# Performance work log

Measured on AMD Instinct MI355X. Metric: run time of the kernel, lower is better.

Reference implementation:

```python
import jax, jax.numpy as jnp
import numpy as np

IOU_THRESHOLD = 0.5  # default iou_threshold of nms/class_spec_nms


def _nms_keep_mask(boxes, scores, iou_threshold):
    """Faithful port of the hand-rolled greedy NMS.

    The torch version builds a variable-length index list; here we return the
    equivalent fixed-shape boolean keep mask over the N boxes (jit-friendly).
    """
    n = scores.shape[0]
    x1, y1, x2, y2 = boxes[:, 0], boxes[:, 1], boxes[:, 2], boxes[:, 3]
    areas = (x2 - x1) * (y2 - y1)                       # [N]
    # pairwise intersection via broadcasted min/max (same math as the matmul-
    # with-ones trick in the source, without materializing the ones matrices)
    xi = jnp.minimum(x2[:, None], x2[None, :]) - jnp.maximum(x1[:, None], x1[None, :])
    yi = jnp.minimum(y2[:, None], y2[None, :]) - jnp.maximum(y1[:, None], y1[None, :])
    inter = jnp.maximum(xi, 0.0) * jnp.maximum(yi, 0.0)  # [N,N]
    iou = inter / (areas[:, None] + areas[None, :] - inter)

    first_max = scores.max()
    first_min = scores.min()
    curr_idx0 = jnp.argmax(scores)

    # carry: (candidate mask, working scores copy, keep mask, curr max, curr idx)
    init = (scores < first_max, scores, jnp.zeros((n,), dtype=bool), first_max, curr_idx0)

    def cond(state):
        mask, _, _, cmax, _ = state
        return jnp.any(mask) & (cmax >= first_min)

    def body(state):
        mask, sc, keep, cmax, cidx = state
        mask = mask & (iou[cidx] <= iou_threshold)   # suppress overlaps with current max
        mask = mask.at[cidx].set(False)
        keep = keep.at[cidx].set(True)               # keep current max
        sc = jnp.where(mask, sc, first_min - 1.0)    # kill suppressed scores
        cidx = jnp.argmax(sc)
        return mask, sc, keep, sc[cidx], cidx

    _, _, keep, _, _ = jax.lax.while_loop(cond, body, init)
    return keep


def setup_inputs() -> dict:
    key = jax.random.key(0)
    k1, k2, k3, k4, k5, k6 = jax.random.split(key, 6)
    N = 4096    # pre-NMS candidate boxes
    L = 16384   # p3 locations for a 1024x1024 image at stride 8 (128*128)
    xy = jax.random.uniform(k1, (N, 2), dtype=jnp.float32) * 900.0
    wh = jax.random.uniform(k2, (N, 2), dtype=jnp.float32) * 100.0 + 1.0
    boxes = jnp.concatenate([xy, xy + wh], axis=1)          # valid x1<x2, y1<y2
    scores = jax.random.uniform(k3, (N,), dtype=jnp.float32)
    class_ids = jax.random.randint(k4, (N,), 0, 80, dtype=jnp.int32)
    locations = jax.random.uniform(k5, (L, 2), dtype=jnp.float32) * 1024.0
    deltas = jax.random.uniform(k6, (L, 4), dtype=jnp.float32)  # positive gt deltas
    return {"boxes": boxes, "scores": scores, "class_ids": class_ids,
            "locations": locations, "deltas": deltas, "stride": 8}


def reference(boxes, scores, class_ids, locations, deltas, stride):
    # ---- class_spec_nms: class-offset trick then plain NMS ----
    max_coordinate = boxes.max()
    offsets = class_ids.astype(boxes.dtype) * (max_coordinate + 1.0)
    boxes_for_nms = boxes + offsets[:, None]
    keep_mask = _nms_keep_mask(boxes_for_nms, scores, IOU_THRESHOLD)

    # ---- fcos_apply_deltas_to_locations ----
    clipped = jnp.maximum(deltas, 0.0)
    s = jnp.asarray(stride, dtype=deltas.dtype)
    px, py = locations[:, 0], locations[:, 1]
    pred_boxes = jnp.stack([px - clipped[:, 0] * s,
                            py - clipped[:, 1] * s,
                            px + clipped[:, 2] * s,
                            py + clipped[:, 3] * s], axis=1)  # [L,4]

    # ---- fcos_make_centerness_targets ----
    lr_min = jnp.minimum(deltas[:, 0], deltas[:, 2])
    tb_min = jnp.minimum(deltas[:, 1], deltas[:, 3])
    lr_max = jnp.maximum(deltas[:, 0], deltas[:, 2])
    tb_max = jnp.maximum(deltas[:, 1], deltas[:, 3])
    centerness = jnp.sqrt((lr_min * tb_min) / (lr_max * tb_max))
    centerness = jnp.where(jnp.all(deltas == -1.0, axis=1), -1.0, centerness)

    pred_out = jnp.concatenate([pred_boxes, centerness[:, None]], axis=1)  # [L,5]
    return keep_mask, pred_out
```

## Files before the change

### kernel.cpp

```cpp
#include <hip/hip_runtime.h>
#include <stdint.h>

#define NB 4096
#define NBLK 64
#define LLOC 16384
#define IOU_THR 0.5f
#define ECAP 1024
#define RANKB 256
#define NTRI (NBLK * (NBLK + 1) / 2)

typedef unsigned long long u64;

__device__ __forceinline__ u64 readlane64(u64 v, int lane) {
    unsigned lo = (unsigned)__builtin_amdgcn_readlane((int)(unsigned)(v & 0xffffffffull), lane);
    unsigned hi = (unsigned)__builtin_amdgcn_readlane((int)(unsigned)(v >> 32), lane);
    return ((u64)hi << 32) | (u64)lo;
}

__global__ void __launch_bounds__(256) fused_front(
        const float* __restrict__ boxes, const float* __restrict__ scores,
        const float* __restrict__ loc, const float* __restrict__ deltas,
        const int* __restrict__ stride_p,
        float* __restrict__ pred_out, float* __restrict__ maxc,
        int* __restrict__ sidx, int* __restrict__ counts) {
    __shared__ __align__(16) float sh[NB];
    __shared__ float red[4];
    int blk = blockIdx.x;
    int t = threadIdx.x;

    if (blk < 64) {
        int i = blk * 256 + t;
        float s = (float)stride_p[0];
        float2 p = ((const float2*)loc)[i];
        float4 d = ((const float4*)deltas)[i];
        float c0 = fmaxf(d.x, 0.f), c1 = fmaxf(d.y, 0.f);
        float c2 = fmaxf(d.z, 0.f), c3 = fmaxf(d.w, 0.f);
        float b0 = p.x - c0 * s;
        float b1 = p.y - c1 * s;
        float b2 = p.x + c2 * s;
        float b3 = p.y + c3 * s;
        float lr_min = fminf(d.x, d.z), tb_min = fminf(d.y, d.w);
        float lr_max = fmaxf(d.x, d.z), tb_max = fmaxf(d.y, d.w);
        float cent = sqrtf((lr_min * tb_min) / (lr_max * tb_max));
        if (d.x == -1.f && d.y == -1.f && d.z == -1.f && d.w == -1.f) cent = -1.f;
        float* o = pred_out + (size_t)i * 5;
        o[0] = b0; o[1] = b1; o[2] = b2; o[3] = b3; o[4] = cent;
    } else if (blk < 64 + RANKB) {
        for (int i = t; i < NB; i += 256) sh[i] = scores[i];
        __syncthreads();
        int wave = t >> 6, lane = t & 63;
        int base = (blk - 64) * 16 + wave * 4;
        float my0 = sh[base + 0], my1 = sh[base + 1];
        float my2 = sh[base + 2], my3 = sh[base + 3];
        int c0 = 0, c1 = 0, c2 = 0, c3 = 0;
#pragma unroll 8
        for (int k = 0; k < 64; ++k) {
            int j = lane + k * 64;
            float sj = sh[j];
            c0 += (sj > my0) || (sj == my0 && j < base + 0);
            c1 += (sj > my1) || (sj == my1 && j < base + 1);
            c2 += (sj > my2) || (sj == my2 && j < base + 2);
            c3 += (sj > my3) || (sj == my3 && j < base + 3);
        }
        for (int o = 32; o > 0; o >>= 1) {
            c0 += __shfl_down(c0, o); c1 += __shfl_down(c1, o);
            c2 += __shfl_down(c2, o); c3 += __shfl_down(c3, o);
        }
        if (lane == 0) {
            sidx[c0] = base + 0; sidx[c1] = base + 1;
            sidx[c2] = base + 2; sidx[c3] = base + 3;
        }
    } else {
        if (t < NBLK) counts[t] = 0;
        float m = -3.0e38f;
        for (int i = t; i < NB * 4; i += 256) m = fmaxf(m, boxes[i]);
        for (int o = 32; o > 0; o >>= 1) m = fmaxf(m, __shfl_down(m, o));
        if ((t & 63) == 0) red[t >> 6] = m;
        __syncthreads();
        if (t == 0) *maxc = fmaxf(fmaxf(red[0], red[1]), fmaxf(red[2], red[3]));
    }
}

__global__ void __launch_bounds__(64) edge_kernel(
        const float* __restrict__ boxes, const int* __restrict__ cls,
        const float* __restrict__ maxc, const int* __restrict__ sidx,
        int* __restrict__ counts, uint4* __restrict__ entries) {
    int idx = blockIdx.x, r = 0;
    while (idx >= NBLK - r) { idx -= NBLK - r; ++r; }
    int c = r + idx;

    __shared__ float4 cb[64];
    __shared__ float ca[64];
    int t = threadIdx.x;
    float mc1 = maxc[0] + 1.0f;

    int jr = sidx[r * 64 + t];
    float offr = (float)cls[jr] * mc1;
    float4 rb = ((const float4*)boxes)[jr];
    rb.x += offr; rb.y += offr; rb.z += offr; rb.w += offr;
    float ra = (rb.z - rb.x) * (rb.w - rb.y);

    if (c == r) {
        cb[t] = rb; ca[t] = ra;
    } else {
        int jc = sidx[c * 64 + t];
        float offc = (float)cls[jc] * mc1;
        float4 b = ((const float4*)boxes)[jc];
        b.x += offc; b.y += offc; b.z += offc; b.w += offc;
        cb[t] = b; ca[t] = (b.z - b.x) * (b.w - b.y);
    }
    __syncthreads();

    u64 w = 0;
#pragma unroll 8
    for (int j = 0; j < 64; ++j) {
        float4 b = cb[j];
        float xi = fminf(rb.z, b.z) - fmaxf(rb.x, b.x);
        float yi = fminf(rb.w, b.w) - fmaxf(rb.y, b.y);
        float inter = fmaxf(xi, 0.f) * fmaxf(yi, 0.f);
        float iou = inter / (ra + ca[j] - inter);
        w |= (u64)(iou > IOU_THR) << j;
    }
    if (c == r) w &= ~(1ull << t);
    if (w) {
        int slot = atomicAdd(&counts[r], 1);
        if (slot < ECAP)
            entries[r * ECAP + slot] =
                make_uint4((unsigned)(t | (c << 8)), 0u,
                           (unsigned)(w & 0xffffffffull), (unsigned)(w >> 32));
    }
}

__global__ void __launch_bounds__(64) scan_kernel(
        const int* __restrict__ counts, const uint4* __restrict__ entries,
        const int* __restrict__ sidx, float* __restrict__ keep_out) {
    const int lane = threadIdx.x;
    int cnt_l = counts[lane];
    u64 accv = 0;
    u64 keptall = 0;
    u64 self = 1ull << lane;

    uint4 cur = entries[lane];
    uint4 n1  = entries[ECAP + lane];
    for (int b = 0; b < NBLK; ++b) {
        uint4 n2;
        if (b < NBLK - 2) n2 = entries[(u64)(b + 2) * ECAP + lane];

        int cnt = __builtin_amdgcn_readlane(cnt_l, b);
        if (cnt > ECAP) cnt = ECAP;
        int cfast = cnt < 64 ? cnt : 64;

        u64 colw = self;
        for (int e = 0; e < cfast; ++e) {
            unsigned meta = (unsigned)__builtin_amdgcn_readlane((int)cur.x, e);
            int l = meta & 255, c = meta >> 8;
            if (c == b) {
                unsigned lo = (unsigned)__builtin_amdgcn_readlane((int)cur.z, e);
                unsigned hi = (unsigned)__builtin_amdgcn_readlane((int)cur.w, e);
                if (lane == l) colw |= ((u64)hi << 32) | lo;
            }
        }
        for (int e = 64; e < cnt; ++e) {
            uint4 x = entries[(u64)b * ECAP + e];
            int l = x.x & 255, c = x.x >> 8;
            if (c == b && lane == l) colw |= ((u64)x.w << 32) | x.z;
        }

        u64 rem = readlane64(accv, b);
        u64 avail = ~rem;
        u64 edges = colw & avail & ~self;
        u64 involved = __ballot(edges != 0ull) & avail;
        u64 keptm = avail & ~involved;
        u64 sub = involved;
        while (sub) {
            int i = (int)__builtin_ctzll(sub);
            keptm |= 1ull << i;
            u64 ci = readlane64(colw, i);
            sub &= ~(ci | (1ull << i));
        }
        if (lane == b) keptall = keptm;

        for (int e = 0; e < cfast; ++e) {
            unsigned meta = (unsigned)__builtin_amdgcn_readlane((int)cur.x, e);
            unsigned lo   = (unsigned)__builtin_amdgcn_readlane((int)cur.z, e);
            unsigned hi   = (unsigned)__builtin_amdgcn_readlane((int)cur.w, e);
            int l = meta & 255, c = meta >> 8;
            if (((keptm >> l) & 1ull) && lane == c) accv |= ((u64)hi << 32) | lo;
        }
        for (int e = 64; e < cnt; ++e) {
            uint4 x = entries[(u64)b * ECAP + e];
            int l = x.x & 255, c = x.x >> 8;
            if (((keptm >> l) & 1ull) && lane == c) accv |= ((u64)x.w << 32) | x.z;
        }
        cur = n1; n1 = n2;
    }

#pragma unroll 8
    for (int bb = 0; bb < NBLK; ++bb) {
        u64 kw = readlane64(keptall, bb);
        int idx = sidx[bb * 64 + lane];
        keep_out[idx] = ((kw >> lane) & 1ull) ? 1.0f : 0.0f;
    }
}

extern "C" void kernel_launch(void* const* d_in, const int* in_sizes, int n_in,
                              void* d_out, int out_size, void* d_ws, size_t ws_size,
                              hipStream_t stream) {
    const float* boxes   = (const float*)d_in[0];
    const float* scores  = (const float*)d_in[1];
    const int*   cls     = (const int*)d_in[2];
    const float* loc     = (const float*)d_in[3];
    const float* deltas  = (const float*)d_in[4];
    const int*   stride  = (const int*)d_in[5];

    float* out = (float*)d_out;
    float* keep_out = out;
    float* pred_out = out + NB;

    char* ws = (char*)d_ws;
    float* maxc    = (float*)ws;                     ws += 16;
    int*   sidx    = (int*)ws;                       ws += NB * sizeof(int);
    int*   counts  = (int*)ws;                       ws += NBLK * sizeof(int) + 16;
    uint4* entries = (uint4*)ws;

    fused_front<<<64 + RANKB + 1, 256, 0, stream>>>(boxes, scores, loc, deltas, stride,
                                                    pred_out, maxc, sidx, counts);
    edge_kernel<<<NTRI, 64, 0, stream>>>(boxes, cls, maxc, sidx, counts, entries);
    scan_kernel<<<1, 64, 0, stream>>>(counts, entries, sidx, keep_out);
}
```

Baseline: 103.8 us.

## Fuse front, edge and scan kernels into one cooperative persistent kernel

The three separate launches (front/rank, pairwise IoU edge tiles, serial scan) are merged into one cooperative kernel with 256 blocks. Grid-wide syncs replace the kernel boundaries. The 2080 edge tiles are spread over the waves of the persistent grid in three rounds, and block 0 wave 0 runs the serial scan at the end. This removes two launch overheads and inter-kernel gaps, but adds grid.sync costs and leaves most of the grid idle during the scan phase.

```diff
diff --git a/kernel.cpp b/kernel.cpp
--- a/kernel.cpp
+++ b/kernel.cpp
@@ -1,13 +1,15 @@
 #include <hip/hip_runtime.h>
+#include <hip/hip_cooperative_groups.h>
 #include <stdint.h>
+
+namespace cg = cooperative_groups;
 
 #define NB 4096
 #define NBLK 64
-#define LLOC 16384
 #define IOU_THR 0.5f
 #define ECAP 1024
-#define RANKB 256
 #define NTRI (NBLK * (NBLK + 1) / 2)
+#define GRID 256
 
 typedef unsigned long long u64;
 
@@ -17,17 +19,48 @@
     return ((u64)hi << 32) | (u64)lo;
 }
 
-__global__ void __launch_bounds__(256) fused_front(
+__global__ void __launch_bounds__(256, 1) fcos_fused(
         const float* __restrict__ boxes, const float* __restrict__ scores,
-        const float* __restrict__ loc, const float* __restrict__ deltas,
-        const int* __restrict__ stride_p,
-        float* __restrict__ pred_out, float* __restrict__ maxc,
-        int* __restrict__ sidx, int* __restrict__ counts) {
+        const int* __restrict__ cls, const float* __restrict__ loc,
+        const float* __restrict__ deltas, const int* __restrict__ stride_p,
+        float* __restrict__ keep_out, float* __restrict__ pred_out,
+        float* __restrict__ maxc, int* __restrict__ sidx,
+        int* __restrict__ counts, uint4* __restrict__ entries) {
+    cg::grid_group grid = cg::this_grid();
     __shared__ __align__(16) float sh[NB];
     __shared__ float red[4];
-    int blk = blockIdx.x;
-    int t = threadIdx.x;
-
+    __shared__ float4 cbs[4][64];
+    __shared__ float  cas[4][64];
+
+    const int blk  = blockIdx.x;
+    const int t    = threadIdx.x;
+    const int wave = t >> 6, lane = t & 63;
+
+    {
+        for (int i = t; i < NB; i += 256) sh[i] = scores[i];
+        __syncthreads();
+        int base = blk * 16 + wave * 4;
+        float my0 = sh[base + 0], my1 = sh[base + 1];
+        float my2 = sh[base + 2], my3 = sh[base + 3];
+        int c0 = 0, c1 = 0, c2 = 0, c3 = 0;
+#pragma unroll 8
+        for (int k = 0; k < 64; ++k) {
+            int j = lane + k * 64;
+            float sj = sh[j];
+            c0 += (sj > my0) || (sj == my0 && j < base + 0);
+            c1 += (sj > my1) || (sj == my1 && j < base + 1);
+            c2 += (sj > my2) || (sj == my2 && j < base + 2);
+            c3 += (sj > my3) || (sj == my3 && j < base + 3);
+        }
+        for (int o = 32; o > 0; o >>= 1) {
+            c0 += __shfl_down(c0, o); c1 += __shfl_down(c1, o);
+            c2 += __shfl_down(c2, o); c3 += __shfl_down(c3, o);
+        }
+        if (lane == 0) {
+            sidx[c0] = base + 0; sidx[c1] = base + 1;
+            sidx[c2] = base + 2; sidx[c3] = base + 3;
+        }
+    }
     if (blk < 64) {
         int i = blk * 256 + t;
         float s = (float)stride_p[0];
@@ -45,32 +78,7 @@
         if (d.x == -1.f && d.y == -1.f && d.z == -1.f && d.w == -1.f) cent = -1.f;
         float* o = pred_out + (size_t)i * 5;
         o[0] = b0; o[1] = b1; o[2] = b2; o[3] = b3; o[4] = cent;
-    } else if (blk < 64 + RANKB) {
-        for (int i = t; i < NB; i += 256) sh[i] = scores[i];
-        __syncthreads();
-        int wave = t >> 6, lane = t & 63;
-        int base = (blk - 64) * 16 + wave * 4;
-        float my0 = sh[base + 0], my1 = sh[base + 1];
-        float my2 = sh[base + 2], my3 = sh[base + 3];
-        int c0 = 0, c1 = 0, c2 = 0, c3 = 0;
-#pragma unroll 8
-        for (int k = 0; k < 64; ++k) {
-            int j = lane + k * 64;
-            float sj = sh[j];
-            c0 += (sj > my0) || (sj == my0 && j < base + 0);
-            c1 += (sj > my1) || (sj == my1 && j < base + 1);
-            c2 += (sj > my2) || (sj == my2 && j < base + 2);
-            c3 += (sj > my3) || (sj == my3 && j < base + 3);
-        }
-        for (int o = 32; o > 0; o >>= 1) {
-            c0 += __shfl_down(c0, o); c1 += __shfl_down(c1, o);
-            c2 += __shfl_down(c2, o); c3 += __shfl_down(c3, o);
-        }
-        if (lane == 0) {
-            sidx[c0] = base + 0; sidx[c1] = base + 1;
-            sidx[c2] = base + 2; sidx[c3] = base + 3;
-        }
-    } else {
+    } else if (blk == 64) {
         if (t < NBLK) counts[t] = 0;
         float m = -3.0e38f;
         for (int i = t; i < NB * 4; i += 256) m = fmaxf(m, boxes[i]);
@@ -79,127 +87,128 @@
         __syncthreads();
         if (t == 0) *maxc = fmaxf(fmaxf(red[0], red[1]), fmaxf(red[2], red[3]));
     }
-}
-
-__global__ void __launch_bounds__(64) edge_kernel(
-        const float* __restrict__ boxes, const int* __restrict__ cls,
-        const float* __restrict__ maxc, const int* __restrict__ sidx,
-        int* __restrict__ counts, uint4* __restrict__ entries) {
-    int idx = blockIdx.x, r = 0;
-    while (idx >= NBLK - r) { idx -= NBLK - r; ++r; }
-    int c = r + idx;
-
-    __shared__ float4 cb[64];
-    __shared__ float ca[64];
-    int t = threadIdx.x;
+    __threadfence();
+    grid.sync();
+
     float mc1 = maxc[0] + 1.0f;
-
-    int jr = sidx[r * 64 + t];
-    float offr = (float)cls[jr] * mc1;
-    float4 rb = ((const float4*)boxes)[jr];
-    rb.x += offr; rb.y += offr; rb.z += offr; rb.w += offr;
-    float ra = (rb.z - rb.x) * (rb.w - rb.y);
-
-    if (c == r) {
-        cb[t] = rb; ca[t] = ra;
-    } else {
-        int jc = sidx[c * 64 + t];
-        float offc = (float)cls[jc] * mc1;
-        float4 b = ((const float4*)boxes)[jc];
-        b.x += offc; b.y += offc; b.z += offc; b.w += offc;
-        cb[t] = b; ca[t] = (b.z - b.x) * (b.w - b.y);
-    }
-    __syncthreads();
-
-    u64 w = 0;
+    for (int round = 0; round < 3; ++round) {
+        int tile = round * (GRID * 4) + blk * 4 + wave;
+        bool active = tile < NTRI;
+        int r = 0, cc = 0;
+        float4 rb; float ra = 0.f;
+        if (active) {
+            int idx = tile;
+            while (idx >= NBLK - r) { idx -= NBLK - r; ++r; }
+            cc = r + idx;
+            int jr = sidx[r * 64 + lane];
+            float offr = (float)cls[jr] * mc1;
+            rb = ((const float4*)boxes)[jr];
+            rb.x += offr; rb.y += offr; rb.z += offr; rb.w += offr;
+            ra = (rb.z - rb.x) * (rb.w - rb.y);
+            if (cc == r) {
+                cbs[wave][lane] = rb; cas[wave][lane] = ra;
+            } else {
+                int jc = sidx[cc * 64 + lane];
+                float offc = (float)cls[jc] * mc1;
+                float4 b = ((const float4*)boxes)[jc];
+                b.x += offc; b.y += offc; b.z += offc; b.w += offc;
+                cbs[wave][lane] = b;
+                cas[wave][lane] = (b.z - b.x) * (b.w - b.y);
+            }
+        }
+        __syncthreads();
+        if (active) {
+            u64 w = 0;
 #pragma unroll 8
-    for (int j = 0; j < 64; ++j) {
-        float4 b = cb[j];
-        float xi = fminf(rb.z, b.z) - fmaxf(rb.x, b.x);
-        float yi = fminf(rb.w, b.w) - fmaxf(rb.y, b.y);
-        float inter = fmaxf(xi, 0.f) * fmaxf(yi, 0.f);
-        float iou = inter / (ra + ca[j] - inter);
-        w |= (u64)(iou > IOU_THR) << j;
-    }
-    if (c == r) w &= ~(1ull << t);
-    if (w) {
-        int slot = atomicAdd(&counts[r], 1);
-        if (slot < ECAP)
-            entries[r * ECAP + slot] =
-                make_uint4((unsigned)(t | (c << 8)), 0u,
-                           (unsigned)(w & 0xffffffffull), (unsigned)(w >> 32));
-    }
-}
-
-__global__ void __launch_bounds__(64) scan_kernel(
-        const int* __restrict__ counts, const uint4* __restrict__ entries,
-        const int* __restrict__ sidx, float* __restrict__ keep_out) {
-    const int lane = threadIdx.x;
-    int cnt_l = counts[lane];
-    u64 accv = 0;
-    u64 keptall = 0;
-    u64 self = 1ull << lane;
-
-    uint4 cur = entries[lane];
-    uint4 n1  = entries[ECAP + lane];
-    for (int b = 0; b < NBLK; ++b) {
-        uint4 n2;
-        if (b < NBLK - 2) n2 = entries[(u64)(b + 2) * ECAP + lane];
-
-        int cnt = __builtin_amdgcn_readlane(cnt_l, b);
-        if (cnt > ECAP) cnt = ECAP;
-        int cfast = cnt < 64 ? cnt : 64;
-
-        u64 colw = self;
-        for (int e = 0; e < cfast; ++e) {
-            unsigned meta = (unsigned)__builtin_amdgcn_readlane((int)cur.x, e);
-            int l = meta & 255, c = meta >> 8;
-            if (c == b) {
-                unsigned lo = (unsigned)__builtin_amdgcn_readlane((int)cur.z, e);
-                unsigned hi = (unsigned)__builtin_amdgcn_readlane((int)cur.w, e);
-                if (lane == l) colw |= ((u64)hi << 32) | lo;
-            }
-        }
-        for (int e = 64; e < cnt; ++e) {
-            uint4 x = entries[(u64)b * ECAP + e];
-            int l = x.x & 255, c = x.x >> 8;
-            if (c == b && lane == l) colw |= ((u64)x.w << 32) | x.z;
-        }
-
-        u64 rem = readlane64(accv, b);
-        u64 avail = ~rem;
-        u64 edges = colw & avail & ~self;
-        u64 involved = __ballot(edges != 0ull) & avail;
-        u64 keptm = avail & ~involved;
-        u64 sub = involved;
-        while (sub) {
-            int i = (int)__builtin_ctzll(sub);
-            keptm |= 1ull << i;
-            u64 ci = readlane64(colw, i);
-            sub &= ~(ci | (1ull << i));
-        }
-        if (lane == b) keptall = keptm;
-
-        for (int e = 0; e < cfast; ++e) {
-            unsigned meta = (unsigned)__builtin_amdgcn_readlane((int)cur.x, e);
-            unsigned lo   = (unsigned)__builtin_amdgcn_readlane((int)cur.z, e);
-            unsigned hi   = (unsigned)__builtin_amdgcn_readlane((int)cur.w, e);
-            int l = meta & 255, c = meta >> 8;
-            if (((keptm >> l) & 1ull) && lane == c) accv |= ((u64)hi << 32) | lo;
-        }
-        for (int e = 64; e < cnt; ++e) {
-            uint4 x = entries[(u64)b * ECAP + e];
-            int l = x.x & 255, c = x.x >> 8;
-            if (((keptm >> l) & 1ull) && lane == c) accv |= ((u64)x.w << 32) | x.z;
-        }
-        cur = n1; n1 = n2;
-    }
+            for (int j = 0; j < 64; ++j) {
+                float4 b = cbs[wave][j];
+                float xi = fminf(rb.z, b.z) - fmaxf(rb.x, b.x);
+                float yi = fminf(rb.w, b.w) - fmaxf(rb.y, b.y);
+                float inter = fmaxf(xi, 0.f) * fmaxf(yi, 0.f);
+                float iou = inter / (ra + cas[wave][j] - inter);
+                w |= (u64)(iou > IOU_THR) << j;
+            }
+            if (cc == r) w &= ~(1ull << lane);
+            if (w) {
+                int slot = atomicAdd(&counts[r], 1);
+                if (slot < ECAP)
+                    entries[r * ECAP + slot] =
+                        make_uint4((unsigned)(lane | (cc << 8)), 0u,
+                                   (unsigned)(w & 0xffffffffull), (unsigned)(w >> 32));
+            }
+        }
+        __syncthreads();
+    }
+    __threadfence();
+    grid.sync();
+
+    if (blk == 0 && wave == 0) {
+        int cnt_l = counts[lane];
+        u64 accv = 0;
+        u64 keptall = 0;
+        u64 self = 1ull << lane;
+
+        uint4 cur = entries[lane];
+        uint4 n1  = entries[ECAP + lane];
+        for (int b = 0; b < NBLK; ++b) {
+            uint4 n2;
+            if (b < NBLK - 2) n2 = entries[(u64)(b + 2) * ECAP + lane];
+
+            int cnt = __builtin_amdgcn_readlane(cnt_l, b);
+            if (cnt > ECAP) cnt = ECAP;
+            int cfast = cnt < 64 ? cnt : 64;
+
+            u64 colw = self;
+            for (int e = 0; e < cfast; ++e) {
+                unsigned meta = (unsigned)__builtin_amdgcn_readlane((int)cur.x, e);
+                int l = meta & 255, c = meta >> 8;
+                if (c == b) {
+                    unsigned lo = (unsigned)__builtin_amdgcn_readlane((int)cur.z, e);
+                    unsigned hi = (unsigned)__builtin_amdgcn_readlane((int)cur.w, e);
+                    if (lane == l) colw |= ((u64)hi << 32) | lo;
+                }
+            }
+            for (int e = 64; e < cnt; ++e) {
+                uint4 x = entries[(u64)b * ECAP + e];
+                int l = x.x & 255, c = x.x >> 8;
+                if (c == b && lane == l) colw |= ((u64)x.w << 32) | x.z;
+            }
+
+            u64 rem = readlane64(accv, b);
+            u64 avail = ~rem;
+            u64 edges = colw & avail & ~self;
+            u64 involved = __ballot(edges != 0ull) & avail;
+            u64 keptm = avail & ~involved;
+            u64 sub = involved;
+            while (sub) {
+                int i = (int)__builtin_ctzll(sub);
+                keptm |= 1ull << i;
+                u64 ci = readlane64(colw, i);
+                sub &= ~(ci | (1ull << i));
+            }
+            if (lane == b) keptall = keptm;
+
+            for (int e = 0; e < cfast; ++e) {
+                unsigned meta = (unsigned)__builtin_amdgcn_readlane((int)cur.x, e);
+                unsigned lo   = (unsigned)__builtin_amdgcn_readlane((int)cur.z, e);
+                unsigned hi   = (unsigned)__builtin_amdgcn_readlane((int)cur.w, e);
+                int l = meta & 255, c = meta >> 8;
+                if (((keptm >> l) & 1ull) && lane == c) accv |= ((u64)hi << 32) | lo;
+            }
+            for (int e = 64; e < cnt; ++e) {
+                uint4 x = entries[(u64)b * ECAP + e];
+                int l = x.x & 255, c = x.x >> 8;
+                if (((keptm >> l) & 1ull) && lane == c) accv |= ((u64)x.w << 32) | x.z;
+            }
+            cur = n1; n1 = n2;
+        }
 
 #pragma unroll 8
-    for (int bb = 0; bb < NBLK; ++bb) {
-        u64 kw = readlane64(keptall, bb);
-        int idx = sidx[bb * 64 + lane];
-        keep_out[idx] = ((kw >> lane) & 1ull) ? 1.0f : 0.0f;
+        for (int bb = 0; bb < NBLK; ++bb) {
+            u64 kw = readlane64(keptall, bb);
+            int idx = sidx[bb * 64 + lane];
+            keep_out[idx] = ((kw >> lane) & 1ull) ? 1.0f : 0.0f;
+        }
     }
 }
 
@@ -223,8 +232,10 @@
     int*   counts  = (int*)ws;                       ws += NBLK * sizeof(int) + 16;
     uint4* entries = (uint4*)ws;
 
-    fused_front<<<64 + RANKB + 1, 256, 0, stream>>>(boxes, scores, loc, deltas, stride,
-                                                    pred_out, maxc, sidx, counts);
-    edge_kernel<<<NTRI, 64, 0, stream>>>(boxes, cls, maxc, sidx, counts, entries);
-    scan_kernel<<<1, 64, 0, stream>>>(counts, entries, sidx, keep_out);
+    void* args[] = { (void*)&boxes, (void*)&scores, (void*)&cls, (void*)&loc,
+                     (void*)&deltas, (void*)&stride, (void*)&keep_out,
+                     (void*)&pred_out, (void*)&maxc, (void*)&sidx,
+                     (void*)&counts, (void*)&entries };
+    hipLaunchCooperativeKernel((const void*)fcos_fused, dim3(GRID), dim3(256),
+                               args, 0, stream);
 }
```

New measurement: 232.6 us. 2.24x slower.
